# Optimization experiments

Hardware: AMD Instinct MI355X
Metric: run time of the kernel (lower is better)

Reference implementation:

```python
import jax, jax.numpy as jnp
import numpy as np
import math

B, S, H, NH = 4, 4096, 1024, 1
HD = H // NH
D_FF = 4 * H
R = 2  # number of causal rules
SPARSITY = 0.9
LN_EPS = 1e-5


def setup_inputs() -> dict:
    key = jax.random.key(0)
    ks = jax.random.split(key, 16)
    n = lambda k, shp, s=0.02: jax.random.normal(k, shp, dtype=jnp.float32) * s
    return {
        "x": jax.random.normal(ks[0], (B, S, H), dtype=jnp.float32),
        "attention_mask": jnp.ones((B, S), dtype=bool),
        # attention projections (torch Linear convention: weight [out, in])
        "wq": n(ks[1], (H, H)), "bq": jnp.zeros((H,), jnp.float32),
        "wk": n(ks[2], (H, H)), "bk": jnp.zeros((H,), jnp.float32),
        "wv": n(ks[3], (H, H)), "bv": jnp.zeros((H,), jnp.float32),
        "wo": n(ks[4], (H, H)), "bo": jnp.zeros((H,), jnp.float32),
        # layer norms
        "ln1_g": jnp.ones((H,), jnp.float32), "ln1_b": jnp.zeros((H,), jnp.float32),
        "ln2_g": jnp.ones((H,), jnp.float32), "ln2_b": jnp.zeros((H,), jnp.float32),
        # sparse FFN
        "fc1_w": n(ks[5], (D_FF, H)), "fc1_b": jnp.zeros((D_FF,), jnp.float32),
        "fc2_w": n(ks[6], (H, D_FF)), "fc2_b": jnp.zeros((H,), jnp.float32),
        "router_w": n(ks[7], (D_FF, H)), "router_b": jnp.zeros((D_FF,), jnp.float32),
        # causal biasing network: per rule, cause extractor Linear(H,1) and effect predictor Linear(1,H)
        "cause_w": n(ks[8], (R, H)), "cause_b": jnp.zeros((R,), jnp.float32),
        "eff_w": n(ks[9], (R, H)), "eff_b": jnp.zeros((R, H), jnp.float32),
        "strengths": jnp.array([0.8, 0.5], dtype=jnp.float32),
    }


def _ln(x, g, b):
    m = jnp.mean(x, axis=-1, keepdims=True)
    v = jnp.mean((x - m) ** 2, axis=-1, keepdims=True)
    return (x - m) / jnp.sqrt(v + LN_EPS) * g + b


def reference(x, attention_mask, wq, bq, wk, bk, wv, bv, wo, bo,
              ln1_g, ln1_b, ln2_g, ln2_b, fc1_w, fc1_b, fc2_w, fc2_b,
              router_w, router_b, cause_w, cause_b, eff_w, eff_b, strengths):
    # --- attention sub-block ---
    h1 = _ln(x, ln1_g, ln1_b)
    q = (jnp.einsum('bsh,oh->bso', h1, wq) + bq).reshape(B, S, NH, HD).transpose(0, 2, 1, 3)
    k = (jnp.einsum('bsh,oh->bso', h1, wk) + bk).reshape(B, S, NH, HD).transpose(0, 2, 1, 3)
    v = (jnp.einsum('bsh,oh->bso', h1, wv) + bv).reshape(B, S, NH, HD).transpose(0, 2, 1, 3)
    scores = jnp.einsum('bhqd,bhkd->bhqk', q, k) / math.sqrt(HD)  # [B,NH,S,S]
    causal = jnp.triu(jnp.ones((S, S), dtype=bool), 1)
    scores = jnp.where(causal[None, None], jnp.float32(-10000.0), scores)
    scores = jnp.where(~attention_mask[:, None, None, :], jnp.float32(-10000.0), scores)
    # rule-based causal bias: sum_r (effect_emb_r @ h1^T)
    cs = jnp.einsum('bsh,rh->rbs', h1, cause_w) + cause_b[:, None, None]      # [R,B,S]
    exp_eff = cs * strengths[:, None, None]                                   # [R,B,S]
    eff = exp_eff[..., None] * eff_w[:, None, None, :] + eff_b[:, None, None, :]  # [R,B,S,H]
    bias = jnp.einsum('rbsh,bth->bst', eff, h1)                               # [B,S,S], sums rules
    bias = bias.reshape(B, S, NH, S).transpose(0, 2, 1, 3)                    # valid since NH==1
    scores = scores + bias
    attn = jax.nn.softmax(scores, axis=-1)
    ctx = jnp.einsum('bhqk,bhkd->bhqd', attn, v).transpose(0, 2, 1, 3).reshape(B, S, H)
    x = x + jnp.einsum('bsh,oh->bso', ctx, wo) + bo
    # --- sparse FFN sub-block ---
    h2 = _ln(x, ln2_g, ln2_b)
    ff = jax.nn.gelu(jnp.einsum('bsh,fh->bsf', h2, fc1_w) + fc1_b, approximate=False)
    logits = jnp.einsum('bsh,fh->bsf', h2, router_w) + router_b
    k_top = max(1, int(D_FF * (1.0 - SPARSITY)))  # 409
    _, idx = jax.lax.top_k(logits.reshape(B * S, D_FF), k_top)
    rows = jnp.arange(B * S)[:, None]
    mask = jnp.zeros((B * S, D_FF), jnp.float32).at[rows, idx].set(1.0).reshape(B, S, D_FF)
    x = x + jnp.einsum('bsf,hf->bsh', ff * mask, fc2_w) + fc2_b
    return (x, attn)
```

## Files before the change

kernel.cpp:

```cpp
#include <hip/hip_runtime.h>


typedef unsigned short ushortT;
typedef short bf16x8 __attribute__((ext_vector_type(8)));
typedef float f32x4 __attribute__((ext_vector_type(4)));
typedef unsigned short us8 __attribute__((ext_vector_type(8)));

#define SEQ 4096
#define HDIM 1024
#define TOK 16384
#define DFF 4096
#define KTOP 409

__device__ __forceinline__ float b2f(unsigned short u) {
    return __uint_as_float(((unsigned)u) << 16);
}
__device__ __forceinline__ unsigned short f2b(float f) {
    unsigned u = __float_as_uint(f);
    u += 0x7fffu + ((u >> 16) & 1u);
    return (unsigned short)(u >> 16);
}

__device__ __forceinline__ float blkRedF(float v, float* red4) {
    #pragma unroll
    for (int o = 32; o; o >>= 1) v += __shfl_xor(v, o);
    if ((threadIdx.x & 63) == 0) red4[threadIdx.x >> 6] = v;
    __syncthreads();
    v = red4[0] + red4[1] + red4[2] + red4[3];
    __syncthreads();
    return v;
}
__device__ __forceinline__ int blkRedI(int v, int* red4) {
    #pragma unroll
    for (int o = 32; o; o >>= 1) v += __shfl_xor(v, o);
    if ((threadIdx.x & 63) == 0) red4[threadIdx.x >> 6] = v;
    __syncthreads();
    v = red4[0] + red4[1] + red4[2] + red4[3];
    __syncthreads();
    return v;
}

template<int HASLO>
__global__ __launch_bounds__(256) void cvt2_k(const float* __restrict__ s,
                                              ushortT* __restrict__ hi,
                                              ushortT* __restrict__ lo) {
    const int i = (blockIdx.x * 256 + threadIdx.x) * 4;
    float4 v = *(const float4*)(s + i);
    float vv[4] = {v.x, v.y, v.z, v.w};
    ushort4 h, l;
    unsigned short* hp = &h.x; unsigned short* lp = &l.x;
    #pragma unroll
    for (int j = 0; j < 4; ++j) {
        hp[j] = f2b(vv[j]);
        if constexpr (HASLO) lp[j] = f2b(vv[j] - b2f(hp[j]));
    }
    *(ushort4*)(hi + i) = h;
    if constexpr (HASLO) *(ushort4*)(lo + i) = l;
}

__global__ __launch_bounds__(256) void ln_k(const float* __restrict__ in,
                                            ushortT* __restrict__ ohi,
                                            ushortT* __restrict__ olo,
                                            const float* __restrict__ g,
                                            const float* __restrict__ b) {
    __shared__ float red4[4];
    const long long row = blockIdx.x;
    const int t = threadIdx.x;
    float4 v = ((const float4*)(in + row * HDIM))[t];
    float x[4] = {v.x, v.y, v.z, v.w};
    float s = x[0] + x[1] + x[2] + x[3];
    s = blkRedF(s, red4);
    const float mean = s * (1.0f / HDIM);
    float vs = 0.f;
    #pragma unroll
    for (int k2 = 0; k2 < 4; ++k2) { float d = x[k2] - mean; vs += d * d; }
    vs = blkRedF(vs, red4);
    const float inv = 1.0f / sqrtf(vs * (1.0f / HDIM) + 1e-5f);
    float4 gv = ((const float4*)g)[t];
    float4 bv = ((const float4*)b)[t];
    float o[4];
    o[0] = (x[0] - mean) * inv * gv.x + bv.x;
    o[1] = (x[1] - mean) * inv * gv.y + bv.y;
    o[2] = (x[2] - mean) * inv * gv.z + bv.z;
    o[3] = (x[3] - mean) * inv * gv.w + bv.w;
    ushort4 h, l;
    unsigned short* hp = &h.x; unsigned short* lp = &l.x;
    #pragma unroll
    for (int j = 0; j < 4; ++j) {
        hp[j] = f2b(o[j]);
        lp[j] = f2b(o[j] - b2f(hp[j]));
    }
    ((ushort4*)(ohi + row * HDIM))[t] = h;
    ((ushort4*)(olo + row * HDIM))[t] = l;
}

__global__ __launch_bounds__(256) void bias_pre(const ushortT* __restrict__ hhi,
        const ushortT* __restrict__ hlo,
        const float* __restrict__ cw, const float* __restrict__ cb,
        const float* __restrict__ ew, const float* __restrict__ eb,
        const float* __restrict__ st,
        float* __restrict__ e0, float* __restrict__ e1,
        float* __restrict__ uu, float* __restrict__ ww, float* __restrict__ zz) {
    const int tok = blockIdx.x * 4 + (threadIdx.x >> 6);
    const int L = threadIdx.x & 63;
    const long long base = (long long)tok * HDIM + L * 16;
    float d0 = 0, d1 = 0, du = 0, dw = 0, dz = 0;
    #pragma unroll
    for (int q = 0; q < 16; ++q) {
        float hv = b2f(hhi[base + q]) + b2f(hlo[base + q]);
        d0 += hv * cw[L * 16 + q];
        d1 += hv * cw[HDIM + L * 16 + q];
        du += hv * ew[L * 16 + q];
        dw += hv * ew[HDIM + L * 16 + q];
        dz += hv * (eb[L * 16 + q] + eb[HDIM + L * 16 + q]);
    }
    #pragma unroll
    for (int o = 32; o; o >>= 1) {
        d0 += __shfl_xor(d0, o); d1 += __shfl_xor(d1, o);
        du += __shfl_xor(du, o); dw += __shfl_xor(dw, o); dz += __shfl_xor(dz, o);
    }
    if (L == 0) {
        e0[tok] = (d0 + cb[0]) * st[0];
        e1[tok] = (d1 + cb[1]) * st[1];
        uu[tok] = du; ww[tok] = dw; zz[tok] = dz;
    }
}

__global__ __launch_bounds__(256) void row_sum(const float* __restrict__ e,
                                               float* __restrict__ l) {
    __shared__ float red4[4];
    const long long row = blockIdx.x;
    const float4* p = (const float4*)(e + row * (long long)SEQ + threadIdx.x * 16);
    float s = 0.f;
    #pragma unroll
    for (int i = 0; i < 4; ++i) {
        float4 v = p[i];
        s += v.x + v.y + v.z + v.w;
    }
    s = blkRedF(s, red4);
    if (threadIdx.x == 0) l[row] = s;
}

__global__ __launch_bounds__(256) void attn_norm(float* __restrict__ attn,
                                                 const float* __restrict__ l) {
    const long long g = (long long)blockIdx.x * 256 + threadIdx.x;
    const long long base = g * 8;
    const float inv = 1.0f / l[base >> 12];
    float4 v0 = *(const float4*)(attn + base);
    float4 v1 = *(const float4*)(attn + base + 4);
    v0.x *= inv; v0.y *= inv; v0.z *= inv; v0.w *= inv;
    v1.x *= inv; v1.y *= inv; v1.z *= inv; v1.w *= inv;
    *(float4*)(attn + base) = v0;
    *(float4*)(attn + base + 4) = v1;
}

__global__ __launch_bounds__(256) void topk_mask(const float* __restrict__ logits,
                                                 ushortT* __restrict__ ff) {
    __shared__ int red4[4];
    __shared__ int sc[256];
    const long long row = blockIdx.x;
    const int t = threadIdx.x;
    const float* lg = logits + row * (long long)DFF + t * 16;
    unsigned key[16];
    #pragma unroll
    for (int q4 = 0; q4 < 4; ++q4) {
        float4 v = ((const float4*)lg)[q4];
        float vv[4] = {v.x, v.y, v.z, v.w};
        #pragma unroll
        for (int j = 0; j < 4; ++j) {
            unsigned u = __float_as_uint(vv[j]);
            key[q4 * 4 + j] = (u & 0x80000000u) ? ~u : (u | 0x80000000u);
        }
    }
    unsigned T = 0;
    for (int bit = 31; bit >= 0; --bit) {
        unsigned cand = T | (1u << bit);
        int c = 0;
        #pragma unroll
        for (int q = 0; q < 16; ++q) c += (key[q] >= cand);
        c = blkRedI(c, red4);
        if (c >= KTOP) T = cand;
    }
    int cg = 0, eq = 0;
    #pragma unroll
    for (int q = 0; q < 16; ++q) { cg += (key[q] > T); eq += (key[q] == T); }
    cg = blkRedI(cg, red4);
    const int need = KTOP - cg;
    sc[t] = eq;
    __syncthreads();
    for (int o = 1; o < 256; o <<= 1) {
        int x = (t >= o) ? sc[t - o] : 0;
        __syncthreads();
        sc[t] += x;
        __syncthreads();
    }
    int pre = sc[t] - eq;
    ushortT* fr = ff + row * (long long)DFF + t * 16;
    #pragma unroll
    for (int q = 0; q < 16; ++q) {
        bool sel = (key[q] > T) || ((key[q] == T) && (pre < need));
        if (key[q] == T) pre++;
        if (!sel) fr[q] = 0;
    }
}

struct GemmP {
    const ushortT* A; const ushortT* A2; const float* Af;
    const ushortT* B; const ushortT* B2;
    long long aBatch, bBatch, oBatch;
    int lda, ldb, K, ldo;
    void* out; void* out2;
    const float* biasN; const float* biasM;
    const float *pe0, *pe1, *pu, *pw, *pz, *pl;
    const float* resF32;
    float scale;
};

template<int EPI, int AMODE, int BMODE>
__global__ __launch_bounds__(256) void gemm_nt(GemmP p) {
    __shared__ ushortT Ahi[4096];
    __shared__ ushortT Bhi[4096];
    __shared__ ushortT Alo[(AMODE >= 2) ? 4096 : 8];
    __shared__ ushortT Blo[(BMODE == 1) ? 4096 : 8];
    const int tid = threadIdx.x;
    const int L = tid & 63;
    const int w = tid >> 6;
    const int wm = w >> 1, wn = w & 1;
    const int bn = blockIdx.x, bm = blockIdx.y, bz = blockIdx.z;

    f32x4 acc[4][4] = {};

    const long long obase = (long long)bz * p.oBatch;
    float* Of = (float*)p.out;
    ushortT* Oh = (ushortT*)p.out;
    ushortT* Ol = (ushortT*)p.out2;

    int gnv[4];
    #pragma unroll
    for (int j = 0; j < 4; ++j) gnv[j] = bn * 128 + wn * 64 + j * 16 + (L & 15);

    if constexpr (EPI == 2) {
        if (bn > bm) {
            #pragma unroll
            for (int i = 0; i < 4; ++i)
                #pragma unroll
                for (int r = 0; r < 4; ++r) {
                    const int gm = bm * 128 + wm * 64 + i * 16 + ((L >> 4) << 2) + r;
                    #pragma unroll
                    for (int j = 0; j < 4; ++j)
                        Of[obase + (long long)gm * p.ldo + gnv[j]] = 0.f;
                }
            return;
        }
    }

    int kEnd = p.K;
    if constexpr (EPI == 3) { kEnd = min(p.K, (bm + 1) * 128); }

    const int r0row = tid >> 2;
    const int r1row = 64 + r0row;
    const int rc   = ((tid & 3) ^ ((tid >> 3) & 3)) * 8;
    const int qsw  = (((L >> 4) ^ ((L >> 1) & 3))) * 8;

    for (int k0 = 0; k0 < kEnd; k0 += 32) {
        if constexpr (AMODE != 2) {
            const ushortT* Ab = p.A + (long long)bz * p.aBatch
                              + (long long)bm * 128 * p.lda + k0 + rc;
            __builtin_amdgcn_global_load_lds(
                (const __attribute__((address_space(1))) void*)(Ab + (long long)r0row * p.lda),
                (__attribute__((address_space(3))) void*)(Ahi + w * 512), 16, 0, 0);
            __builtin_amdgcn_global_load_lds(
                (const __attribute__((address_space(1))) void*)(Ab + (long long)r1row * p.lda),
                (__attribute__((address_space(3))) void*)(Ahi + 2048 + w * 512), 16, 0, 0);
            if constexpr (AMODE == 3) {
                const ushortT* Ab2 = p.A2 + (long long)bz * p.aBatch
                                   + (long long)bm * 128 * p.lda + k0 + rc;
                __builtin_amdgcn_global_load_lds(
                    (const __attribute__((address_space(1))) void*)(Ab2 + (long long)r0row * p.lda),
                    (__attribute__((address_space(3))) void*)(Alo + w * 512), 16, 0, 0);
                __builtin_amdgcn_global_load_lds(
                    (const __attribute__((address_space(1))) void*)(Ab2 + (long long)r1row * p.lda),
                    (__attribute__((address_space(3))) void*)(Alo + 2048 + w * 512), 16, 0, 0);
            }
        } else {
            const int arow = tid >> 1;
            const float* ap = p.Af + (long long)bz * p.aBatch
                            + ((long long)bm * 128 + arow) * p.lda
                            + k0 + (tid & 1) * 16;
            #pragma unroll
            for (int cc = 0; cc < 2; ++cc) {
                const int c = (tid & 1) * 2 + cc;
                const int cs = (c ^ ((arow >> 1) & 3)) * 8;
                float4 v0 = ((const float4*)ap)[cc * 2];
                float4 v1 = ((const float4*)ap)[cc * 2 + 1];
                float vv[8] = {v0.x, v0.y, v0.z, v0.w, v1.x, v1.y, v1.z, v1.w};
                us8 h, l;
                #pragma unroll
                for (int j = 0; j < 8; ++j) {
                    h[j] = f2b(vv[j]);
                    l[j] = f2b(vv[j] - b2f(h[j]));
                }
                *(us8*)(Ahi + arow * 32 + cs) = h;
                *(us8*)(Alo + arow * 32 + cs) = l;
            }
        }
        {
            const ushortT* Bb = p.B + (long long)bz * p.bBatch
                              + (long long)bn * 128 * p.ldb + k0 + rc;
            __builtin_amdgcn_global_load_lds(
                (const __attribute__((address_space(1))) void*)(Bb + (long long)r0row * p.ldb),
                (__attribute__((address_space(3))) void*)(Bhi + w * 512), 16, 0, 0);
            __builtin_amdgcn_global_load_lds(
                (const __attribute__((address_space(1))) void*)(Bb + (long long)r1row * p.ldb),
                (__attribute__((address_space(3))) void*)(Bhi + 2048 + w * 512), 16, 0, 0);
            if constexpr (BMODE == 1) {
                const ushortT* Bb2 = p.B2 + (long long)bz * p.bBatch
                                   + (long long)bn * 128 * p.ldb + k0 + rc;
                __builtin_amdgcn_global_load_lds(
                    (const __attribute__((address_space(1))) void*)(Bb2 + (long long)r0row * p.ldb),
                    (__attribute__((address_space(3))) void*)(Blo + w * 512), 16, 0, 0);
                __builtin_amdgcn_global_load_lds(
                    (const __attribute__((address_space(1))) void*)(Bb2 + (long long)r1row * p.ldb),
                    (__attribute__((address_space(3))) void*)(Blo + 2048 + w * 512), 16, 0, 0);
            }
        }
        __syncthreads();
        {
            bf16x8 ah[4], bh[4];
            #pragma unroll
            for (int i = 0; i < 4; ++i)
                ah[i] = *(const bf16x8*)(Ahi + (wm * 64 + i * 16 + (L & 15)) * 32 + qsw);
            #pragma unroll
            for (int j = 0; j < 4; ++j)
                bh[j] = *(const bf16x8*)(Bhi + (wn * 64 + j * 16 + (L & 15)) * 32 + qsw);
            #pragma unroll
            for (int i = 0; i < 4; ++i)
                #pragma unroll
                for (int j = 0; j < 4; ++j)
                    acc[i][j] = __builtin_amdgcn_mfma_f32_16x16x32_bf16(ah[i], bh[j], acc[i][j], 0, 0, 0);
            if constexpr (BMODE == 1) {
                bf16x8 bl[4];
                #pragma unroll
                for (int j = 0; j < 4; ++j)
                    bl[j] = *(const bf16x8*)(Blo + (wn * 64 + j * 16 + (L & 15)) * 32 + qsw);
                #pragma unroll
                for (int i = 0; i < 4; ++i)
                    #pragma unroll
                    for (int j = 0; j < 4; ++j)
                        acc[i][j] = __builtin_amdgcn_mfma_f32_16x16x32_bf16(ah[i], bl[j], acc[i][j], 0, 0, 0);
            }
            if constexpr (AMODE >= 2) {
                bf16x8 al[4];
                #pragma unroll
                for (int i = 0; i < 4; ++i)
                    al[i] = *(const bf16x8*)(Alo + (wm * 64 + i * 16 + (L & 15)) * 32 + qsw);
                #pragma unroll
                for (int i = 0; i < 4; ++i)
                    #pragma unroll
                    for (int j = 0; j < 4; ++j)
                        acc[i][j] = __builtin_amdgcn_mfma_f32_16x16x32_bf16(al[i], bh[j], acc[i][j], 0, 0, 0);
            }
        }
        __syncthreads();
    }

    float c0[4], c1[4], c2[4];
    #pragma unroll
    for (int j = 0; j < 4; ++j) {
        if constexpr (EPI == 2) {
            c0[j] = p.pu[bz * SEQ + gnv[j]];
            c1[j] = p.pw[bz * SEQ + gnv[j]];
            c2[j] = p.pz[bz * SEQ + gnv[j]];
        } else if constexpr (EPI == 4 || EPI == 5 || EPI == 6 || EPI == 9) {
            c0[j] = p.biasN[gnv[j]];
        }
    }

    #pragma unroll
    for (int i = 0; i < 4; ++i) {
        #pragma unroll
        for (int r = 0; r < 4; ++r) {
            const int gm = bm * 128 + wm * 64 + i * 16 + ((L >> 4) << 2) + r;
            float rA = 0.f, rB = 0.f, mult = 1.f;
            if constexpr (EPI == 2) { rA = p.pe0[bz * SEQ + gm]; rB = p.pe1[bz * SEQ + gm]; }
            if constexpr (EPI == 3) mult = 1.0f / p.pl[bz * SEQ + gm];
            if constexpr (EPI == 8) rA = p.biasM[gm];
            #pragma unroll
            for (int j = 0; j < 4; ++j) {
                float v = acc[i][j][r];
                const long long oidx = obase + (long long)gm * p.ldo + gnv[j];
                if constexpr (EPI == 2) {
                    float s = v * p.scale + rA * c0[j] + rB * c1[j] + c2[j];
                    Of[oidx] = (gnv[j] <= gm) ? __expf(s) : 0.f;
                } else if constexpr (EPI == 3) {
                    float val = v * mult;
                    ushortT h = f2b(val);
                    Oh[oidx] = h; Ol[oidx] = f2b(val - b2f(h));
                } else if constexpr (EPI == 4) {
                    Of[oidx] = v + c0[j] + p.resF32[(long long)gm * p.ldo + gnv[j]];
                } else if constexpr (EPI == 5) {
                    float tt = v + c0[j];
                    Oh[oidx] = f2b(0.5f * tt * (1.0f + erff(tt * 0.70710678118654752f)));
                } else if constexpr (EPI == 6) {
                    float val = v + c0[j];
                    ushortT h = f2b(val);
                    Oh[oidx] = h; Ol[oidx] = f2b(val - b2f(h));
                } else if constexpr (EPI == 8) {
                    float val = v + rA;
                    ushortT h = f2b(val);
                    Oh[oidx] = h; Ol[oidx] = f2b(val - b2f(h));
                } else if constexpr (EPI == 9) {
                    Of[oidx] = v + c0[j];
                }
            }
        }
    }
}

extern "C" void kernel_launch(void* const* d_in, const int* in_sizes, int n_in,
                              void* d_out, int out_size, void* d_ws, size_t ws_size,
                              hipStream_t stream) {
    (void)in_sizes; (void)n_in; (void)out_size; (void)ws_size;
    const float* x    = (const float*)d_in[0];
    const float* wq   = (const float*)d_in[2];
    const float* bq   = (const float*)d_in[3];
    const float* wk   = (const float*)d_in[4];
    const float* bk   = (const float*)d_in[5];
    const float* wv   = (const float*)d_in[6];
    const float* bv   = (const float*)d_in[7];
    const float* wo   = (const float*)d_in[8];
    const float* bo   = (const float*)d_in[9];
    const float* ln1g = (const float*)d_in[10];
    const float* ln1b = (const float*)d_in[11];
    const float* ln2g = (const float*)d_in[12];
    const float* ln2b = (const float*)d_in[13];
    const float* fc1w = (const float*)d_in[14];
    const float* fc1b = (const float*)d_in[15];
    const float* fc2w = (const float*)d_in[16];
    const float* fc2b = (const float*)d_in[17];
    const float* rww  = (const float*)d_in[18];
    const float* rwb  = (const float*)d_in[19];
    const float* cw   = (const float*)d_in[20];
    const float* cb   = (const float*)d_in[21];
    const float* ew   = (const float*)d_in[22];
    const float* eb   = (const float*)d_in[23];
    const float* st   = (const float*)d_in[24];

    char* ws = (char*)d_ws;
    const size_t MB32 = 33554432;
    ushortT* h1hi = (ushortT*)(ws + 0 * MB32);
    ushortT* h1lo = (ushortT*)(ws + 1 * MB32);
    ushortT* qhi  = (ushortT*)(ws + 2 * MB32);
    ushortT* qlo  = (ushortT*)(ws + 3 * MB32);
    ushortT* khi  = (ushortT*)(ws + 4 * MB32);
    ushortT* klo  = (ushortT*)(ws + 5 * MB32);
    ushortT* vthi = (ushortT*)(ws + 6 * MB32);
    ushortT* vtlo = (ushortT*)(ws + 7 * MB32);
    ushortT* ctxhi = qhi;
    ushortT* ctxlo = qlo;
    float*   x1   = (float*)(ws + 0 * MB32);
    ushortT* h2hi = khi;
    ushortT* h2lo = klo;
    ushortT* fw   = vthi;
    float*   logc = (float*)(ws + 2 * MB32);
    ushortT* ffc  = (ushortT*)(ws + 7 * MB32);
    char* tail = ws + 8 * MB32;
    ushortT* whi = (ushortT*)(tail);
    ushortT* wlo = (ushortT*)(tail + 2097152);
    char* sm = tail + 4194304;
    float* e0v = (float*)(sm);
    float* e1v = (float*)(sm + 1 * 65536);
    float* uu  = (float*)(sm + 2 * 65536);
    float* wwp = (float*)(sm + 3 * 65536);
    float* zz  = (float*)(sm + 4 * 65536);
    float* lrow = (float*)(sm + 5 * 65536);

    const int NW = HDIM * HDIM;
    const int NF = DFF * HDIM;
    ushortT* fc1h = fw;
    ushortT* fc2h = fw + 1 * (size_t)NF;
    ushortT* rwh  = fw + 2 * (size_t)NF;
    ushortT* rwl  = fw + 3 * (size_t)NF;

    float* outx = (float*)d_out;
    float* attn = outx + (size_t)TOK * HDIM;

    ln_k<<<TOK, 256, 0, stream>>>(x, h1hi, h1lo, ln1g, ln1b);

    cvt2_k<1><<<NW / 1024, 256, 0, stream>>>(wq, whi, wlo);
    GemmP pq{};
    pq.A = h1hi; pq.A2 = h1lo; pq.B = whi; pq.B2 = wlo;
    pq.lda = HDIM; pq.ldb = HDIM; pq.K = HDIM; pq.ldo = HDIM;
    pq.out = qhi; pq.out2 = qlo; pq.biasN = bq;
    gemm_nt<6, 3, 1><<<dim3(8, 128, 1), 256, 0, stream>>>(pq);

    cvt2_k<1><<<NW / 1024, 256, 0, stream>>>(wk, whi, wlo);
    pq.out = khi; pq.out2 = klo; pq.biasN = bk;
    gemm_nt<6, 3, 1><<<dim3(8, 128, 1), 256, 0, stream>>>(pq);

    cvt2_k<1><<<NW / 1024, 256, 0, stream>>>(wv, whi, wlo);
    GemmP pv{};
    pv.A = whi; pv.A2 = wlo; pv.B = h1hi; pv.B2 = h1lo;
    pv.lda = HDIM; pv.ldb = HDIM; pv.K = HDIM; pv.ldo = SEQ;
    pv.aBatch = 0; pv.bBatch = (long long)SEQ * HDIM; pv.oBatch = (long long)HDIM * SEQ;
    pv.out = vthi; pv.out2 = vtlo; pv.biasM = bv;
    gemm_nt<8, 3, 1><<<dim3(32, 8, 4), 256, 0, stream>>>(pv);

    bias_pre<<<4096, 256, 0, stream>>>(h1hi, h1lo, cw, cb, ew, eb, st, e0v, e1v, uu, wwp, zz);

    GemmP ps{};
    ps.A = qhi; ps.A2 = qlo; ps.B = khi; ps.B2 = klo;
    ps.lda = HDIM; ps.ldb = HDIM; ps.K = HDIM; ps.ldo = SEQ;
    ps.aBatch = (long long)SEQ * HDIM; ps.bBatch = (long long)SEQ * HDIM;
    ps.oBatch = (long long)SEQ * SEQ;
    ps.out = attn; ps.scale = 0.03125f;
    ps.pe0 = e0v; ps.pe1 = e1v; ps.pu = uu; ps.pw = wwp; ps.pz = zz;
    gemm_nt<2, 3, 1><<<dim3(32, 32, 4), 256, 0, stream>>>(ps);

    row_sum<<<TOK, 256, 0, stream>>>(attn, lrow);

    GemmP pp{};
    pp.Af = attn; pp.B = vthi; pp.B2 = vtlo;
    pp.lda = SEQ; pp.ldb = SEQ; pp.K = SEQ; pp.ldo = HDIM;
    pp.aBatch = (long long)SEQ * SEQ; pp.bBatch = (long long)HDIM * SEQ;
    pp.oBatch = (long long)SEQ * HDIM;
    pp.out = ctxhi; pp.out2 = ctxlo; pp.pl = lrow;
    gemm_nt<3, 2, 1><<<dim3(8, 32, 4), 256, 0, stream>>>(pp);

    attn_norm<<<32768, 256, 0, stream>>>(attn, lrow);

    cvt2_k<1><<<NW / 1024, 256, 0, stream>>>(wo, whi, wlo);
    GemmP po{};
    po.A = ctxhi; po.A2 = ctxlo; po.B = whi; po.B2 = wlo;
    po.lda = HDIM; po.ldb = HDIM; po.K = HDIM; po.ldo = HDIM;
    po.out = x1; po.biasN = bo; po.resF32 = x;
    gemm_nt<4, 3, 1><<<dim3(8, 128, 1), 256, 0, stream>>>(po);

    ln_k<<<TOK, 256, 0, stream>>>(x1, h2hi, h2lo, ln2g, ln2b);

    cvt2_k<0><<<NF / 1024, 256, 0, stream>>>(fc1w, fc1h, nullptr);
    cvt2_k<0><<<NF / 1024, 256, 0, stream>>>(fc2w, fc2h, nullptr);
    cvt2_k<1><<<NF / 1024, 256, 0, stream>>>(rww, rwh, rwl);

    for (int c = 0; c < 4; ++c) {
        const size_t roff = (size_t)c * 4096 * HDIM;
        GemmP pf{};
        pf.A = h2hi + roff; pf.B = fc1h;
        pf.lda = HDIM; pf.ldb = HDIM; pf.K = HDIM; pf.ldo = DFF;
        pf.out = ffc; pf.biasN = fc1b;
        gemm_nt<5, 0, 0><<<dim3(32, 32, 1), 256, 0, stream>>>(pf);

        GemmP pr{};
        pr.A = h2hi + roff; pr.A2 = h2lo + roff; pr.B = rwh; pr.B2 = rwl;
        pr.lda = HDIM; pr.ldb = HDIM; pr.K = HDIM; pr.ldo = DFF;
        pr.out = logc; pr.biasN = rwb;
        gemm_nt<9, 3, 1><<<dim3(32, 32, 1), 256, 0, stream>>>(pr);

        topk_mask<<<4096, 256, 0, stream>>>(logc, ffc);

        GemmP p2{};
        p2.A = ffc; p2.B = fc2h; p2.lda = DFF; p2.ldb = DFF; p2.K = DFF; p2.ldo = HDIM;
        p2.out = outx + roff; p2.biasN = fc2b;
        p2.resF32 = x1 + roff;
        gemm_nt<4, 0, 0><<<dim3(8, 32, 1), 256, 0, stream>>>(p2);
    }
}
```

Baseline: 3.034 ms.

## Fuse Q/K projections, swizzle GEMM block order, skip causal-upper work in softmax passes

```diff
diff --git a/kernel.cpp b/kernel.cpp
--- a/kernel.cpp
+++ b/kernel.cpp
@@ -104,15 +104,24 @@
     const int tok = blockIdx.x * 4 + (threadIdx.x >> 6);
     const int L = threadIdx.x & 63;
     const long long base = (long long)tok * HDIM + L * 16;
+    us8 h0 = *(const us8*)(hhi + base);
+    us8 h1v = *(const us8*)(hhi + base + 8);
+    us8 l0 = *(const us8*)(hlo + base);
+    us8 l1v = *(const us8*)(hlo + base + 8);
+    float hv[16];
+    #pragma unroll
+    for (int q = 0; q < 8; ++q) {
+        hv[q] = b2f(h0[q]) + b2f(l0[q]);
+        hv[8 + q] = b2f(h1v[q]) + b2f(l1v[q]);
+    }
     float d0 = 0, d1 = 0, du = 0, dw = 0, dz = 0;
     #pragma unroll
     for (int q = 0; q < 16; ++q) {
-        float hv = b2f(hhi[base + q]) + b2f(hlo[base + q]);
-        d0 += hv * cw[L * 16 + q];
-        d1 += hv * cw[HDIM + L * 16 + q];
-        du += hv * ew[L * 16 + q];
-        dw += hv * ew[HDIM + L * 16 + q];
-        dz += hv * (eb[L * 16 + q] + eb[HDIM + L * 16 + q]);
+        d0 += hv[q] * cw[L * 16 + q];
+        d1 += hv[q] * cw[HDIM + L * 16 + q];
+        du += hv[q] * ew[L * 16 + q];
+        dw += hv[q] * ew[HDIM + L * 16 + q];
+        dz += hv[q] * (eb[L * 16 + q] + eb[HDIM + L * 16 + q]);
     }
     #pragma unroll
     for (int o = 32; o; o >>= 1) {
@@ -129,27 +138,58 @@
 __global__ __launch_bounds__(256) void row_sum(const float* __restrict__ e,
                                                float* __restrict__ l) {
     __shared__ float red4[4];
-    const long long row = blockIdx.x;
-    const float4* p = (const float4*)(e + row * (long long)SEQ + threadIdx.x * 16);
-    float s = 0.f;
-    #pragma unroll
-    for (int i = 0; i < 4; ++i) {
-        float4 v = p[i];
-        s += v.x + v.y + v.z + v.w;
-    }
-    s = blkRedF(s, red4);
-    if (threadIdx.x == 0) l[row] = s;
+    const int r = blockIdx.x;
+    const int s = r & 4095;
+    const float* rowp = e + (long long)r * SEQ;
+    const int c0 = threadIdx.x * 16;
+    float sum = 0.f;
+    if (c0 + 15 <= s) {
+        const float4* p = (const float4*)(rowp + c0);
+        #pragma unroll
+        for (int i = 0; i < 4; ++i) {
+            float4 v = p[i];
+            sum += v.x + v.y + v.z + v.w;
+        }
+    } else if (c0 <= s) {
+        #pragma unroll
+        for (int i = 0; i < 4; ++i) {
+            float q0 = (c0 + i * 4 + 0 <= s) ? rowp[c0 + i * 4 + 0] : 0.f;
+            float q1 = (c0 + i * 4 + 1 <= s) ? rowp[c0 + i * 4 + 1] : 0.f;
+            float q2 = (c0 + i * 4 + 2 <= s) ? rowp[c0 + i * 4 + 2] : 0.f;
+            float q3 = (c0 + i * 4 + 3 <= s) ? rowp[c0 + i * 4 + 3] : 0.f;
+            sum += q0 + q1 + q2 + q3;
+        }
+    }
+    sum = blkRedF(sum, red4);
+    if (threadIdx.x == 0) l[r] = sum;
 }
 
 __global__ __launch_bounds__(256) void attn_norm(float* __restrict__ attn,
                                                  const float* __restrict__ l) {
     const long long g = (long long)blockIdx.x * 256 + threadIdx.x;
     const long long base = g * 8;
-    const float inv = 1.0f / l[base >> 12];
+    const int r = (int)(base >> 12);
+    const int s = r & 4095;
+    const int c = (int)(base & 4095);
+    float4 z = {0.f, 0.f, 0.f, 0.f};
+    if (c > s) {
+        *(float4*)(attn + base) = z;
+        *(float4*)(attn + base + 4) = z;
+        return;
+    }
+    const float inv = 1.0f / l[r];
     float4 v0 = *(const float4*)(attn + base);
     float4 v1 = *(const float4*)(attn + base + 4);
-    v0.x *= inv; v0.y *= inv; v0.z *= inv; v0.w *= inv;
-    v1.x *= inv; v1.y *= inv; v1.z *= inv; v1.w *= inv;
+    if (c + 7 <= s) {
+        v0.x *= inv; v0.y *= inv; v0.z *= inv; v0.w *= inv;
+        v1.x *= inv; v1.y *= inv; v1.z *= inv; v1.w *= inv;
+    } else {
+        float vv[8] = {v0.x, v0.y, v0.z, v0.w, v1.x, v1.y, v1.z, v1.w};
+        #pragma unroll
+        for (int j = 0; j < 8; ++j) vv[j] = (c + j <= s) ? vv[j] * inv : 0.f;
+        v0.x = vv[0]; v0.y = vv[1]; v0.z = vv[2]; v0.w = vv[3];
+        v1.x = vv[4]; v1.y = vv[5]; v1.z = vv[6]; v1.w = vv[7];
+    }
     *(float4*)(attn + base) = v0;
     *(float4*)(attn + base + 4) = v1;
 }
@@ -210,10 +250,11 @@
     long long aBatch, bBatch, oBatch;
     int lda, ldb, K, ldo;
     void* out; void* out2;
-    const float* biasN; const float* biasM;
+    const float* biasN; const float* biasN2; const float* biasM;
     const float *pe0, *pe1, *pu, *pw, *pz, *pl;
     const float* resF32;
     float scale;
+    int nSplit;
 };
 
 template<int EPI, int AMODE, int BMODE>
@@ -226,7 +267,17 @@
     const int L = tid & 63;
     const int w = tid >> 6;
     const int wm = w >> 1, wn = w & 1;
-    const int bn = blockIdx.x, bm = blockIdx.y, bz = blockIdx.z;
+    int bn = blockIdx.x, bm = blockIdx.y;
+    const int bz = blockIdx.z;
+    {
+        const int nx = gridDim.x;
+        const int n = nx * gridDim.y;
+        if ((n & 7) == 0) {
+            const int id = bm * nx + bn;
+            const int nid = (id & 7) * (n >> 3) + (id >> 3);
+            bn = nid % nx; bm = nid / nx;
+        }
+    }
 
     f32x4 acc[4][4] = {};
 
@@ -240,18 +291,7 @@
     for (int j = 0; j < 4; ++j) gnv[j] = bn * 128 + wn * 64 + j * 16 + (L & 15);
 
     if constexpr (EPI == 2) {
-        if (bn > bm) {
-            #pragma unroll
-            for (int i = 0; i < 4; ++i)
-                #pragma unroll
-                for (int r = 0; r < 4; ++r) {
-                    const int gm = bm * 128 + wm * 64 + i * 16 + ((L >> 4) << 2) + r;
-                    #pragma unroll
-                    for (int j = 0; j < 4; ++j)
-                        Of[obase + (long long)gm * p.ldo + gnv[j]] = 0.f;
-                }
-            return;
-        }
+        if (bn > bm) return;
     }
 
     int kEnd = p.K;
@@ -371,7 +411,10 @@
             c0[j] = p.pu[bz * SEQ + gnv[j]];
             c1[j] = p.pw[bz * SEQ + gnv[j]];
             c2[j] = p.pz[bz * SEQ + gnv[j]];
-        } else if constexpr (EPI == 4 || EPI == 5 || EPI == 6 || EPI == 9) {
+        } else if constexpr (EPI == 6) {
+            c0[j] = (gnv[j] < p.nSplit) ? p.biasN[gnv[j]]
+                                        : p.biasN2[gnv[j] - p.nSplit];
+        } else if constexpr (EPI == 4 || EPI == 5 || EPI == 9) {
             c0[j] = p.biasN[gnv[j]];
         }
     }
@@ -450,17 +493,17 @@
     const size_t MB32 = 33554432;
     ushortT* h1hi = (ushortT*)(ws + 0 * MB32);
     ushortT* h1lo = (ushortT*)(ws + 1 * MB32);
-    ushortT* qhi  = (ushortT*)(ws + 2 * MB32);
-    ushortT* qlo  = (ushortT*)(ws + 3 * MB32);
-    ushortT* khi  = (ushortT*)(ws + 4 * MB32);
-    ushortT* klo  = (ushortT*)(ws + 5 * MB32);
+    ushortT* qkhi = (ushortT*)(ws + 2 * MB32);
+    ushortT* qklo = (ushortT*)(ws + 4 * MB32);
     ushortT* vthi = (ushortT*)(ws + 6 * MB32);
     ushortT* vtlo = (ushortT*)(ws + 7 * MB32);
-    ushortT* ctxhi = qhi;
-    ushortT* ctxlo = qlo;
+    ushortT* wqkh = (ushortT*)(ws + 6 * MB32);
+    ushortT* wqkl = wqkh + 2 * (size_t)(HDIM * HDIM);
+    ushortT* ctxhi = (ushortT*)(ws + 2 * MB32);
+    ushortT* ctxlo = (ushortT*)(ws + 3 * MB32);
     float*   x1   = (float*)(ws + 0 * MB32);
-    ushortT* h2hi = khi;
-    ushortT* h2lo = klo;
+    ushortT* h2hi = (ushortT*)(ws + 4 * MB32);
+    ushortT* h2lo = (ushortT*)(ws + 5 * MB32);
     ushortT* fw   = vthi;
     float*   logc = (float*)(ws + 2 * MB32);
     ushortT* ffc  = (ushortT*)(ws + 7 * MB32);
@@ -487,16 +530,14 @@
 
     ln_k<<<TOK, 256, 0, stream>>>(x, h1hi, h1lo, ln1g, ln1b);
 
-    cvt2_k<1><<<NW / 1024, 256, 0, stream>>>(wq, whi, wlo);
+    cvt2_k<1><<<NW / 1024, 256, 0, stream>>>(wq, wqkh, wqkl);
+    cvt2_k<1><<<NW / 1024, 256, 0, stream>>>(wk, wqkh + NW, wqkl + NW);
     GemmP pq{};
-    pq.A = h1hi; pq.A2 = h1lo; pq.B = whi; pq.B2 = wlo;
-    pq.lda = HDIM; pq.ldb = HDIM; pq.K = HDIM; pq.ldo = HDIM;
-    pq.out = qhi; pq.out2 = qlo; pq.biasN = bq;
-    gemm_nt<6, 3, 1><<<dim3(8, 128, 1), 256, 0, stream>>>(pq);
-
-    cvt2_k<1><<<NW / 1024, 256, 0, stream>>>(wk, whi, wlo);
-    pq.out = khi; pq.out2 = klo; pq.biasN = bk;
-    gemm_nt<6, 3, 1><<<dim3(8, 128, 1), 256, 0, stream>>>(pq);
+    pq.A = h1hi; pq.A2 = h1lo; pq.B = wqkh; pq.B2 = wqkl;
+    pq.lda = HDIM; pq.ldb = HDIM; pq.K = HDIM; pq.ldo = 2048;
+    pq.out = qkhi; pq.out2 = qklo;
+    pq.biasN = bq; pq.biasN2 = bk; pq.nSplit = 1024;
+    gemm_nt<6, 3, 1><<<dim3(16, 128, 1), 256, 0, stream>>>(pq);
 
     cvt2_k<1><<<NW / 1024, 256, 0, stream>>>(wv, whi, wlo);
     GemmP pv{};
@@ -509,9 +550,9 @@
     bias_pre<<<4096, 256, 0, stream>>>(h1hi, h1lo, cw, cb, ew, eb, st, e0v, e1v, uu, wwp, zz);
 
     GemmP ps{};
-    ps.A = qhi; ps.A2 = qlo; ps.B = khi; ps.B2 = klo;
-    ps.lda = HDIM; ps.ldb = HDIM; ps.K = HDIM; ps.ldo = SEQ;
-    ps.aBatch = (long long)SEQ * HDIM; ps.bBatch = (long long)SEQ * HDIM;
+    ps.A = qkhi; ps.A2 = qklo; ps.B = qkhi + 1024; ps.B2 = qklo + 1024;
+    ps.lda = 2048; ps.ldb = 2048; ps.K = HDIM; ps.ldo = SEQ;
+    ps.aBatch = (long long)SEQ * 2048; ps.bBatch = (long long)SEQ * 2048;
     ps.oBatch = (long long)SEQ * SEQ;
     ps.out = attn; ps.scale = 0.03125f;
     ps.pe0 = e0v; ps.pe1 = e1v; ps.pu = uu; ps.pw = wwp; ps.pz = zz;
```

Result: slower. 3.106 ms (+2.4%).
